# Kernel optimization log

Measured on AMD Instinct MI355X. Metric: run time of the kernel, lower is better.

## Reference

```python
import jax, jax.numpy as jnp
import numpy as np

N = 524288   # total points across all events
H = 128      # MLP hidden width
B = 1024     # number of batches (events)


def setup_inputs() -> dict:
    key = jax.random.key(0)
    ks = jax.random.split(key, 6)
    # features[:,0] = per-point input mean, features[:,1] = per-point input std (>0)
    mean = jax.random.normal(ks[0], (N, 1), dtype=jnp.float32)
    std = jax.random.uniform(ks[1], (N, 1), dtype=jnp.float32) * 0.5 + 0.1
    features = jnp.concatenate([mean, std], axis=1)            # [N,2]
    batch_ids = jax.random.randint(ks[2], (N,), 0, B).astype(jnp.int32)
    s = 1.0 / np.sqrt(H).astype(np.float32)
    W1 = jax.random.normal(ks[3], (1, H), dtype=jnp.float32)
    b1 = jnp.zeros((H,), jnp.float32)
    W2 = jax.random.normal(ks[4], (H, H), dtype=jnp.float32) * s
    b2 = jnp.zeros((H,), jnp.float32)
    W3 = jax.random.normal(ks[5], (H, 1), dtype=jnp.float32) * s
    b3 = jnp.zeros((1,), jnp.float32)
    return {"features": features, "batch_ids": batch_ids,
            "W1": W1, "b1": b1, "W2": W2, "b2": b2, "W3": W3, "b3": b3,
            "num_batches": B}


def reference(features, batch_ids, W1, b1, W2, b2, W3, b3, num_batches):
    x0 = features[:, :1]        # [N,1] input means (x.features in the original)
    inpt_std = features[:, 1]   # [N]   input stds
    n = x0.shape[0]
    counts = jnp.maximum(
        jax.ops.segment_sum(jnp.ones((n,), x0.dtype), batch_ids,
                            num_segments=num_batches), 1.0)      # [B]

    def net(x):
        # pointwise MLP then global average pool per batch -> one scalar per event
        h = jnp.tanh(x @ W1 + b1)        # [N,H]
        h = jnp.tanh(h @ W2 + b2)        # [N,H]
        s = (h @ W3 + b3)[:, 0]          # [N]
        return jax.ops.segment_sum(s, batch_ids, num_segments=num_batches) / counts  # [B]

    pred_mean, vjp_fn = jax.vjp(net, x0)
    # d pred[b] / d x_j is nonzero only for points j in batch b (pointwise net +
    # per-batch pool), so ONE VJP with a ones cotangent yields every per-batch
    # Jacobian row simultaneously -- collapsing the original per-batch
    # torch.autograd.grad loop into a single backward pass.
    jac = vjp_fn(jnp.ones_like(pred_mean))[0][:, 0]              # [N]
    # var_b = jac_b^T diag(std_b^2) jac_b = sum_{j in b} std_j^2 * jac_j^2
    pred_sdp_var = jax.ops.segment_sum(inpt_std ** 2 * jac ** 2, batch_ids,
                                       num_segments=num_batches)  # [B]
    return jnp.stack([pred_mean, pred_sdp_var], axis=1)           # [B,2]
```

## Files before the change

### kernel.cpp

```cpp
#include <hip/hip_runtime.h>


#define HH   128
#define NB   1024
#define TBL  4096
#define XMIN (-8.0f)
#define XMAX (8.0f)
#define EPB  16
#define BUILD_BLOCKS (TBL / EPB)
#define MAIN_BLOCKS  256

__global__ __launch_bounds__(256) void build_table_kernel(
    const float* __restrict__ W1, const float* __restrict__ b1,
    const float* __restrict__ W2, const float* __restrict__ b2,
    const float* __restrict__ W3, const float* __restrict__ b3,
    float* __restrict__ s_tab, float* __restrict__ d_tab,
    float* __restrict__ acc)
{
    __shared__ float W2s[HH * HH];
    __shared__ float hus[HH * 2 * EPB];
    const int tid = threadIdx.x;
    {
        const float4* src = (const float4*)W2;
        float4* dst = (float4*)W2s;
        for (int i = tid; i < HH * HH / 4; i += 256) dst[i] = src[i];
    }
    if (blockIdx.x == 0) {
        for (int i = tid; i < 3 * NB; i += 256) acc[i] = 0.0f;
    }
    const float dxt = (XMAX - XMIN) / (float)(TBL - 1);
    const int ebase = blockIdx.x * EPB;
    for (int i = tid; i < EPB * HH; i += 256) {
        int e = i & (EPB - 1);
        int k = i >> 4;
        float x = XMIN + (float)(ebase + e) * dxt;
        float w1 = W1[k];
        float h = tanhf(fmaf(x, w1, b1[k]));
        hus[k * (2 * EPB) + 2 * e]     = h;
        hus[k * (2 * EPB) + 2 * e + 1] = w1 * (1.0f - h * h);
    }
    __syncthreads();

    const int q = tid & 31;
    const int r = tid >> 5;
    const int jb = q * 4;
    float z0[4] = {0,0,0,0}, v0[4] = {0,0,0,0};
    float z1[4] = {0,0,0,0}, v1[4] = {0,0,0,0};
    #pragma unroll 4
    for (int k = 0; k < HH; ++k) {
        float4 w  = *(const float4*)&W2s[k * HH + jb];
        float4 hu = *(const float4*)&hus[k * (2 * EPB) + 4 * r];
        z0[0] = fmaf(hu.x, w.x, z0[0]); z0[1] = fmaf(hu.x, w.y, z0[1]);
        z0[2] = fmaf(hu.x, w.z, z0[2]); z0[3] = fmaf(hu.x, w.w, z0[3]);
        v0[0] = fmaf(hu.y, w.x, v0[0]); v0[1] = fmaf(hu.y, w.y, v0[1]);
        v0[2] = fmaf(hu.y, w.z, v0[2]); v0[3] = fmaf(hu.y, w.w, v0[3]);
        z1[0] = fmaf(hu.z, w.x, z1[0]); z1[1] = fmaf(hu.z, w.y, z1[1]);
        z1[2] = fmaf(hu.z, w.z, z1[2]); z1[3] = fmaf(hu.z, w.w, z1[3]);
        v1[0] = fmaf(hu.w, w.x, v1[0]); v1[1] = fmaf(hu.w, w.y, v1[1]);
        v1[2] = fmaf(hu.w, w.z, v1[2]); v1[3] = fmaf(hu.w, w.w, v1[3]);
    }
    float ps0 = 0.f, pd0 = 0.f, ps1 = 0.f, pd1 = 0.f;
    #pragma unroll
    for (int i = 0; i < 4; ++i) {
        int j = jb + i;
        float b2j = b2[j], w3 = W3[j];
        float h2 = tanhf(z0[i] + b2j);
        ps0 = fmaf(w3, h2, ps0);
        pd0 = fmaf((1.0f - h2 * h2) * w3, v0[i], pd0);
        float h2b = tanhf(z1[i] + b2j);
        ps1 = fmaf(w3, h2b, ps1);
        pd1 = fmaf((1.0f - h2b * h2b) * w3, v1[i], pd1);
    }
    #pragma unroll
    for (int o = 16; o > 0; o >>= 1) {
        ps0 += __shfl_down(ps0, o, 32); pd0 += __shfl_down(pd0, o, 32);
        ps1 += __shfl_down(ps1, o, 32); pd1 += __shfl_down(pd1, o, 32);
    }
    if (q == 0) {
        float bb = b3[0];
        int e = ebase + 2 * r;
        s_tab[e]     = ps0 + bb;  d_tab[e]     = pd0;
        s_tab[e + 1] = ps1 + bb;  d_tab[e + 1] = pd1;
    }
}

__global__ __launch_bounds__(256) void main_pass_kernel(
    const float2* __restrict__ feat, const int* __restrict__ ids,
    const float* __restrict__ s_tab, const float* __restrict__ d_tab,
    float* __restrict__ acc, int n)
{
    __shared__ float ts[TBL];
    __shared__ float td[TBL];
    __shared__ float bs[NB];
    __shared__ float bv[NB];
    __shared__ float bc[NB];
    const int tid = threadIdx.x;
    {
        const float4* s4 = (const float4*)s_tab;
        const float4* d4 = (const float4*)d_tab;
        float4* t4 = (float4*)ts;
        float4* u4 = (float4*)td;
        for (int i = tid; i < TBL / 4; i += 256) { t4[i] = s4[i]; u4[i] = d4[i]; }
    }
    for (int i = tid; i < NB; i += 256) { bs[i] = 0.f; bv[i] = 0.f; bc[i] = 0.f; }
    __syncthreads();
    const float inv_dx = (float)(TBL - 1) / (XMAX - XMIN);
    const int stride = MAIN_BLOCKS * 256;
    for (int i = blockIdx.x * 256 + tid; i < n; i += stride) {
        float2 f = feat[i];
        int b = ids[i];
        float u = (fminf(fmaxf(f.x, XMIN), XMAX) - XMIN) * inv_dx;
        int i0 = (int)u;
        i0 = min(max(i0, 1), TBL - 3);
        float t = u - (float)i0;
        float t2 = t * t, t3 = t2 * t;
        float wm = -0.5f * t3 + t2 - 0.5f * t;
        float w0 =  1.5f * t3 - 2.5f * t2 + 1.0f;
        float w1 = -1.5f * t3 + 2.0f * t2 + 0.5f * t;
        float w2 =  0.5f * t3 - 0.5f * t2;
        float s = wm * ts[i0 - 1] + w0 * ts[i0] + w1 * ts[i0 + 1] + w2 * ts[i0 + 2];
        float d = wm * td[i0 - 1] + w0 * td[i0] + w1 * td[i0 + 1] + w2 * td[i0 + 2];
        atomicAdd(&bs[b], s);
        atomicAdd(&bv[b], f.y * f.y * d * d);
        atomicAdd(&bc[b], 1.0f);
    }
    __syncthreads();
    for (int b = tid; b < NB; b += 256) {
        float c = bc[b];
        if (c != 0.f) {
            atomicAdd(&acc[b], bs[b]);
            atomicAdd(&acc[NB + b], bv[b]);
            atomicAdd(&acc[2 * NB + b], c);
        }
    }
}

__global__ __launch_bounds__(256) void finalize_kernel(const float* __restrict__ acc,
                                                       float* __restrict__ out) {
    int b = blockIdx.x * 256 + threadIdx.x;
    if (b < NB) {
        float c = fmaxf(acc[2 * NB + b], 1.0f);
        out[2 * b]     = acc[b] / c;
        out[2 * b + 1] = acc[NB + b] / (c * c);
    }
}

extern "C" void kernel_launch(void* const* d_in, const int* in_sizes, int n_in,
                              void* d_out, int out_size, void* d_ws, size_t ws_size,
                              hipStream_t stream) {
    const float* feat = (const float*)d_in[0];
    const int*   ids  = (const int*)d_in[1];
    const float* W1   = (const float*)d_in[2];
    const float* b1   = (const float*)d_in[3];
    const float* W2   = (const float*)d_in[4];
    const float* b2   = (const float*)d_in[5];
    const float* W3   = (const float*)d_in[6];
    const float* b3   = (const float*)d_in[7];
    const int n = in_sizes[1];

    float* s_tab = (float*)d_ws;
    float* d_tab = s_tab + TBL;
    float* acc   = d_tab + TBL;

    build_table_kernel<<<BUILD_BLOCKS, 256, 0, stream>>>(W1, b1, W2, b2, W3, b3,
                                                         s_tab, d_tab, acc);
    main_pass_kernel<<<MAIN_BLOCKS, 256, 0, stream>>>((const float2*)feat, ids,
                                                      s_tab, d_tab, acc, n);
    finalize_kernel<<<(NB + 255) / 256, 256, 0, stream>>>(acc, (float*)d_out);
}
```

Measured before the change: 101.8 us.

## Shrink lookup table to 1024 entries and remap build thread tiling

Cuts the interpolation table from 4096 to 1024 samples and processes 4 entries per build block. Each wavefront of 64 threads now handles one table entry with two output columns per thread and a 64-wide shuffle reduction, instead of 32-lane groups covering two entries with four columns each. This reduces build work and the amount of table data each main-pass block loads into shared memory. The coarser table makes the cubic interpolation less accurate, and each build block still copies all of W2 into shared memory.

```diff
diff --git a/kernel.cpp b/kernel.cpp
--- a/kernel.cpp
+++ b/kernel.cpp
@@ -3,10 +3,10 @@
 
 #define HH   128
 #define NB   1024
-#define TBL  4096
+#define TBL  1024
 #define XMIN (-8.0f)
 #define XMAX (8.0f)
-#define EPB  16
+#define EPB  4
 #define BUILD_BLOCKS (TBL / EPB)
 #define MAIN_BLOCKS  256
 
@@ -32,7 +32,7 @@
     const int ebase = blockIdx.x * EPB;
     for (int i = tid; i < EPB * HH; i += 256) {
         int e = i & (EPB - 1);
-        int k = i >> 4;
+        int k = i >> 2;
         float x = XMIN + (float)(ebase + e) * dxt;
         float w1 = W1[k];
         float h = tanhf(fmaf(x, w1, b1[k]));
@@ -41,46 +41,32 @@
     }
     __syncthreads();
 
-    const int q = tid & 31;
-    const int r = tid >> 5;
-    const int jb = q * 4;
-    float z0[4] = {0,0,0,0}, v0[4] = {0,0,0,0};
-    float z1[4] = {0,0,0,0}, v1[4] = {0,0,0,0};
-    #pragma unroll 4
+    const int q = tid & 63;
+    const int r = tid >> 6;
+    const int jb = q * 2;
+    float z0 = 0.f, z1 = 0.f, v0 = 0.f, v1 = 0.f;
+    #pragma unroll 8
     for (int k = 0; k < HH; ++k) {
-        float4 w  = *(const float4*)&W2s[k * HH + jb];
-        float4 hu = *(const float4*)&hus[k * (2 * EPB) + 4 * r];
-        z0[0] = fmaf(hu.x, w.x, z0[0]); z0[1] = fmaf(hu.x, w.y, z0[1]);
-        z0[2] = fmaf(hu.x, w.z, z0[2]); z0[3] = fmaf(hu.x, w.w, z0[3]);
-        v0[0] = fmaf(hu.y, w.x, v0[0]); v0[1] = fmaf(hu.y, w.y, v0[1]);
-        v0[2] = fmaf(hu.y, w.z, v0[2]); v0[3] = fmaf(hu.y, w.w, v0[3]);
-        z1[0] = fmaf(hu.z, w.x, z1[0]); z1[1] = fmaf(hu.z, w.y, z1[1]);
-        z1[2] = fmaf(hu.z, w.z, z1[2]); z1[3] = fmaf(hu.z, w.w, z1[3]);
-        v1[0] = fmaf(hu.w, w.x, v1[0]); v1[1] = fmaf(hu.w, w.y, v1[1]);
-        v1[2] = fmaf(hu.w, w.z, v1[2]); v1[3] = fmaf(hu.w, w.w, v1[3]);
+        float2 w  = *(const float2*)&W2s[k * HH + jb];
+        float2 hu = *(const float2*)&hus[k * (2 * EPB) + 2 * r];
+        z0 = fmaf(hu.x, w.x, z0); z1 = fmaf(hu.x, w.y, z1);
+        v0 = fmaf(hu.y, w.x, v0); v1 = fmaf(hu.y, w.y, v1);
     }
-    float ps0 = 0.f, pd0 = 0.f, ps1 = 0.f, pd1 = 0.f;
+    float b2a = b2[jb], b2b = b2[jb + 1];
+    float w3a = W3[jb], w3b = W3[jb + 1];
+    float h2a = tanhf(z0 + b2a);
+    float h2b = tanhf(z1 + b2b);
+    float ps = fmaf(w3a, h2a, w3b * h2b);
+    float pd = fmaf((1.0f - h2a * h2a) * w3a, v0,
+                    (1.0f - h2b * h2b) * w3b * v1);
     #pragma unroll
-    for (int i = 0; i < 4; ++i) {
-        int j = jb + i;
-        float b2j = b2[j], w3 = W3[j];
-        float h2 = tanhf(z0[i] + b2j);
-        ps0 = fmaf(w3, h2, ps0);
-        pd0 = fmaf((1.0f - h2 * h2) * w3, v0[i], pd0);
-        float h2b = tanhf(z1[i] + b2j);
-        ps1 = fmaf(w3, h2b, ps1);
-        pd1 = fmaf((1.0f - h2b * h2b) * w3, v1[i], pd1);
-    }
-    #pragma unroll
-    for (int o = 16; o > 0; o >>= 1) {
-        ps0 += __shfl_down(ps0, o, 32); pd0 += __shfl_down(pd0, o, 32);
-        ps1 += __shfl_down(ps1, o, 32); pd1 += __shfl_down(pd1, o, 32);
+    for (int o = 32; o > 0; o >>= 1) {
+        ps += __shfl_down(ps, o, 64);
+        pd += __shfl_down(pd, o, 64);
     }
     if (q == 0) {
-        float bb = b3[0];
-        int e = ebase + 2 * r;
-        s_tab[e]     = ps0 + bb;  d_tab[e]     = pd0;
-        s_tab[e + 1] = ps1 + bb;  d_tab[e + 1] = pd1;
+        s_tab[ebase + r] = ps + b3[0];
+        d_tab[ebase + r] = pd;
     }
 }
 
```

Result: faster. 95.91 us (-5.8%).
